# Optimization experiments

Measured on AMD Instinct MI355X. Metric: run time of the kernel, lower is better.

Reference implementation:

```python
import jax, jax.numpy as jnp
import numpy as np
from jax import lax

RESO = 64
PAD = 0.1
PLANES = ('xz', 'xy', 'yz')
_AX = {'xz': (0, 2), 'xy': (0, 1), 'yz': (1, 2)}


def _normalize(p, plane):
    a, b = _AX[plane]
    xy = jnp.stack([p[..., a], p[..., b]], axis=-1)
    xy = (xy + 0.5) / (1.0 + PAD + 1e-6)
    return jnp.clip(xy, 0.0, 1.0 - 1e-6)


def _coord2index(xy):
    xi = (xy * RESO).astype(jnp.int32)
    return xi[..., 0] + RESO * xi[..., 1]  # [B,N]


def _scatter_mean(feat, idx):  # feat [B,N,C], idx [B,N] -> [B,RESO^2,C]
    R2 = RESO * RESO
    def one(f, i):
        s = jnp.zeros((R2, f.shape[-1]), f.dtype).at[i].add(f)
        cnt = jnp.zeros((R2,), f.dtype).at[i].add(1.0)
        return s / jnp.maximum(cnt, 1.0)[:, None]
    return jax.vmap(one)(feat, idx)


def _resblock(x, W0, b0, W1, b1, Ws):
    h = jax.nn.relu(x @ W0.T + b0)
    dx = jax.nn.relu(h @ W1.T + b1)
    return x @ Ws.T + dx


def _conv(x, W, b):
    y = lax.conv_general_dilated(x, W, (1, 1), 'SAME', dimension_numbers=('NCHW', 'OIHW', 'NCHW'))
    return y + b[None, :, None, None]


def _grid_sample_border(fea, grid):
    # fea [B,C,H,W], grid [B,N,2] with (x->W, y->H) in [-1,1]; bilinear, border padding, align_corners=False
    B, C, H, W = fea.shape
    x = jnp.clip(((grid[..., 0] + 1.0) * W - 1.0) * 0.5, 0.0, W - 1.0)
    y = jnp.clip(((grid[..., 1] + 1.0) * H - 1.0) * 0.5, 0.0, H - 1.0)
    x0 = jnp.floor(x); y0 = jnp.floor(y)
    wx = (x - x0)[:, None, :]; wy = (y - y0)[:, None, :]
    x0i = x0.astype(jnp.int32); y0i = y0.astype(jnp.int32)
    x1i = jnp.minimum(x0i + 1, W - 1); y1i = jnp.minimum(y0i + 1, H - 1)
    flat = fea.reshape(B, C, H * W)
    g = lambda yi, xi: jnp.take_along_axis(flat, (yi * W + xi)[:, None, :], axis=2)  # [B,C,N]
    return (g(y0i, x0i) * (1 - wx) * (1 - wy) + g(y0i, x1i) * wx * (1 - wy)
            + g(y1i, x0i) * (1 - wx) * wy + g(y1i, x1i) * wx * wy)


def setup_inputs() -> dict:
    key = jax.random.key(0)
    ks = jax.random.split(key, 16)
    B, N, Nq, H, F = 4, 30000, 30000, 64, 256
    nrm = lambda k, sh, s: jax.random.normal(k, sh, jnp.float32) * s
    return {
        'p': jax.random.uniform(ks[0], (B, N, 3), jnp.float32, -0.5, 0.5),
        'query': jax.random.uniform(ks[1], (B, Nq, 3), jnp.float32, 0.0, 1.0),
        'fc_pos_W': nrm(ks[2], (2 * H, 3), 0.3),
        'fc_pos_b': jnp.zeros((2 * H,), jnp.float32),
        'blk_fc0_W': nrm(ks[3], (3, H, 2 * H), 0.08),
        'blk_fc0_b': jnp.zeros((3, H), jnp.float32),
        'blk_fc1_W': nrm(ks[4], (3, H, H), 0.1),
        'blk_fc1_b': jnp.zeros((3, H), jnp.float32),
        'blk_sc_W': nrm(ks[5], (3, H, 2 * H), 0.08),
        'fc_c_W': nrm(ks[6], (F, H), 0.1),
        'fc_c_b': jnp.zeros((F,), jnp.float32),
        'conv1_W': nrm(ks[7], (F, F, 3, 3), 0.02),
        'conv1_b': jnp.zeros((F,), jnp.float32),
        'conv2_W': nrm(ks[8], (F, F, 3, 3), 0.02),
        'conv2_b': jnp.zeros((F,), jnp.float32),
    }


def reference(p, query, fc_pos_W, fc_pos_b, blk_fc0_W, blk_fc0_b, blk_fc1_W, blk_fc1_b, blk_sc_W, fc_c_W, fc_c_b, conv1_W, conv1_b, conv2_W, conv2_b):
    # point-wise MLP with local pooling (scatter_mean to xz bins, gather back)
    net = p @ fc_pos_W.T + fc_pos_b                  # [B,N,2H]
    net = _resblock(net, blk_fc0_W[0], blk_fc0_b[0], blk_fc1_W[0], blk_fc1_b[0], blk_sc_W[0])  # [B,N,H]
    idx_xz = _coord2index(_normalize(p, 'xz'))       # [B,N]
    for i in (1, 2):
        binmean = _scatter_mean(net, idx_xz)         # [B,R2,H]
        pooled = jnp.take_along_axis(binmean, idx_xz[..., None], axis=1)  # [B,N,H]
        net = jnp.concatenate([net, pooled], axis=-1)
        net = _resblock(net, blk_fc0_W[i], blk_fc0_b[i], blk_fc1_W[i], blk_fc1_b[i], blk_sc_W[i])
    c = net @ fc_c_W.T + fc_c_b                      # [B,N,F]

    B = p.shape[0]
    F = fc_c_W.shape[0]
    out = 0.0
    for plane in PLANES:
        idx = _coord2index(_normalize(p, plane))
        fea = _scatter_mean(c, idx)                  # [B,R2,F]
        fea = fea.transpose(0, 2, 1).reshape(B, F, RESO, RESO)  # H axis = coord1, W axis = coord0
        fea = jax.nn.relu(_conv(fea, conv1_W, conv1_b))
        fea = jax.nn.relu(_conv(fea, conv2_W, conv2_b))
        a, b = _AX[plane]
        grid = jnp.stack([query[..., a], query[..., b]], axis=-1) * 2.0 - 1.0
        out = out + _grid_sample_border(fea, grid)   # [B,F,Nq]
    return out.transpose(0, 2, 1)                    # [B,Nq,F]
```

## Files before the change

### kernel.cpp

```cpp
#include <hip/hip_runtime.h>

#define NPTS 30000
#define PSTR 30208
#define BB 4
#define R2 4096
#define NIMG 12

typedef __attribute__((ext_vector_type(8))) short short8;
typedef __attribute__((ext_vector_type(4))) float floatx4;

__device__ __forceinline__ ushort f2bf(float x){
    union { float f; unsigned u; } v; v.f = x;
    unsigned r = (v.u + 0x7fffu + ((v.u >> 16) & 1u)) >> 16;
    return (ushort)r;
}
__device__ __forceinline__ float bf2f(ushort u){
    union { unsigned u; float f; } v; v.u = ((unsigned)u) << 16; return v.f;
}
__device__ __forceinline__ int p64i(int k){ return (k & 3)*16 + (k >> 2); }

__device__ __forceinline__ int coord_bin(float v){
    float t = (v + 0.5f) / 1.100001f;
    t = fminf(fmaxf(t, 0.0f), 0.999999f);
    return (int)(t * 64.0f);
}

__device__ __forceinline__ void gl_lds16(const ushort* g, ushort* l){
    __builtin_amdgcn_global_load_lds(
        (const __attribute__((address_space(1))) void*)g,
        (__attribute__((address_space(3))) void*)l, 16, 0, 0);
}

__global__ void k_prep(const float* __restrict__ fc_pos_W, const float* __restrict__ fc_pos_b,
                       const float* __restrict__ blk0W, const float* __restrict__ blk1W,
                       const float* __restrict__ blkSW, const float* __restrict__ fccW,
                       const float* __restrict__ c1W, const float* __restrict__ c2W,
                       float* __restrict__ WposTp, float* __restrict__ bposP,
                       ushort* __restrict__ Wcat, ushort* __restrict__ W1p,
                       ushort* __restrict__ Wcp,
                       ushort* __restrict__ WB1, ushort* __restrict__ WB2){
    int t = blockIdx.x*256 + threadIdx.x;
    if (t < 384){ int d = t/128, s = t%128;
        int j = (s<64)? p64i(s) : 64 + p64i(s-64);
        WposTp[t] = fc_pos_W[j*3 + d]; return; }
    t -= 384;
    if (t < 128){ int j = (t<64)? p64i(t) : 64 + p64i(t-64);
        bposP[t] = fc_pos_b[j]; return; }
    t -= 128;
    if (t < 49152){
        int i = t/16384, r = t%16384, n = r/128, kp = r%128;
        int ci = (kp<64)? p64i(kp) : 64 + p64i(kp-64);
        float v = (n<64)? blk0W[(i*64+n)*128 + ci] : blkSW[(i*64+(n-64))*128 + ci];
        Wcat[t] = f2bf(v); return; }
    t -= 49152;
    if (t < 12288){
        int i = t/4096, r = t%4096, n = r/64, kp = r%64;
        W1p[t] = f2bf(blk1W[(i*64+n)*64 + p64i(kp)]); return; }
    t -= 12288;
    if (t < 16384){
        int n = t/64, kp = t%64;
        Wcp[t] = f2bf(fccW[n*64 + p64i(kp)]); return; }
    t -= 16384;
    if (t < 589824){
        int e = t & 7; int rest = t >> 3; int ko = rest & 255; int g5 = rest >> 8;
        int qq = g5 & 3; int kc = (g5 >> 2) & 1; int cc = (g5 >> 3) & 3; int tap = g5 >> 5;
        int kp = cc*64 + kc*32 + qq*8 + e;
        int ci = 64*(kp>>6) + p64i(kp & 63);
        WB1[t] = f2bf(c1W[(ko*256+ci)*9 + tap]); return; }
    t -= 589824;
    if (t < 589824){
        int e = t & 7; int rest = t >> 3; int ko = rest & 255; int g5 = rest >> 8;
        int qq = g5 & 3; int kc = (g5 >> 2) & 1; int cc = (g5 >> 3) & 3; int tap = g5 >> 5;
        int kp = cc*64 + kc*32 + qq*8 + e;
        WB2[t] = f2bf(c2W[(ko*256+kp)*9 + tap]); return; }
}

__global__ void k_net0(const float* __restrict__ p, const float* __restrict__ WposTp,
                       const float* __restrict__ bposP,
                       ushort* __restrict__ NET0, int* __restrict__ IDX){
    int pt = blockIdx.x*256 + threadIdx.x;
    int b = blockIdx.y;
    if (pt >= NPTS) return;
    const float* pp = p + ((long)b*NPTS + pt)*3;
    float p0 = pp[0], p1 = pp[1], p2 = pp[2];
    int c0 = coord_bin(p0), c1 = coord_bin(p1), c2 = coord_bin(p2);
    IDX[(0*BB + b)*NPTS + pt] = c0 + 64*c2;
    IDX[(1*BB + b)*NPTS + pt] = c0 + 64*c1;
    IDX[(2*BB + b)*NPTS + pt] = c1 + 64*c2;
    ushort* out = NET0 + ((long)b*PSTR + pt)*128;
    #pragma unroll
    for (int s = 0; s < 128; s += 4){
        ushort4 v;
        v.x = f2bf(bposP[s+0] + p0*WposTp[s+0] + p1*WposTp[128+s+0] + p2*WposTp[256+s+0]);
        v.y = f2bf(bposP[s+1] + p0*WposTp[s+1] + p1*WposTp[128+s+1] + p2*WposTp[256+s+1]);
        v.z = f2bf(bposP[s+2] + p0*WposTp[s+2] + p1*WposTp[128+s+2] + p2*WposTp[256+s+2]);
        v.w = f2bf(bposP[s+3] + p0*WposTp[s+3] + p1*WposTp[128+s+3] + p2*WposTp[256+s+3]);
        *(ushort4*)(out + s) = v;
    }
}

__global__ void k_qbin(const float* __restrict__ query, int* __restrict__ qIDX){
    int t = blockIdx.x*256 + threadIdx.x;
    if (t >= BB*NPTS) return;
    const float* qp = query + (long)t*3;
    int x = min((int)(fmaxf(qp[0], 0.0f)*16.0f), 15);
    int y = min((int)(fmaxf(qp[1], 0.0f)*16.0f), 15);
    int z = min((int)(fmaxf(qp[2], 0.0f)*16.0f), 15);
    qIDX[t] = (x<<8) | (y<<4) | z;
}

__global__ void k_hist(const int* __restrict__ IDX, int* __restrict__ hist, int n){
    int t = blockIdx.x*256 + threadIdx.x;
    if (t >= n) return;
    int img = t / NPTS;
    atomicAdd(&hist[img*R2 + IDX[t]], 1);
}

__global__ void k_scan(const int* __restrict__ hist, int* __restrict__ binStart,
                       int* __restrict__ cursor){
    __shared__ int sums[256];
    int img = blockIdx.x; int tid = threadIdx.x;
    int v[16]; int s = 0;
    const int* h = hist + img*R2 + tid*16;
    #pragma unroll
    for (int i=0;i<16;i++){ v[i] = s; s += h[i]; }
    sums[tid] = s;
    __syncthreads();
    for (int d=1; d<256; d<<=1){
        int t = (tid>=d)? sums[tid-d] : 0;
        __syncthreads();
        sums[tid] += t;
        __syncthreads();
    }
    int base = (tid==0)? 0 : sums[tid-1];
    int* bs = binStart + img*R2 + tid*16;
    int* cu = cursor  + img*R2 + tid*16;
    #pragma unroll
    for (int i=0;i<16;i++){ bs[i] = base + v[i]; cu[i] = base + v[i]; }
}

__global__ void k_mklist(const int* __restrict__ IDX, int* __restrict__ cursor,
                         int* __restrict__ plist, int n){
    int t = blockIdx.x*256 + threadIdx.x;
    if (t >= n) return;
    int img = t / NPTS; int pt = t - img*NPTS;
    int bin = IDX[t];
    int pos = atomicAdd(&cursor[img*R2 + bin], 1);
    plist[img*NPTS + pos] = pt;
}

__global__ void __launch_bounds__(256) k_res_mfma(
        const ushort* __restrict__ X1, const ushort* __restrict__ X2, int s1, int s2,
        const ushort* __restrict__ Wcat, const float* __restrict__ b0,
        const ushort* __restrict__ W1p, const float* __restrict__ b1,
        ushort* __restrict__ Y){
    __shared__ __align__(16) ushort lds[4][64*72];
    int tid = threadIdx.x, lane = tid & 63, w = tid >> 6;
    int m16 = lane & 15, q = lane >> 4;
    int b = blockIdx.y;
    int pt0 = blockIdx.x*256 + w*64;
    const ushort* x1 = X1 + (long)b*PSTR*s1;
    const ushort* x2 = X2 + (long)b*PSTR*s2;
    floatx4 accH[4][4], accS[4][4];
    #pragma unroll
    for (int nt=0; nt<4; nt++){
        float bv = b0[nt*16 + m16];
        #pragma unroll
        for (int mt=0; mt<4; mt++){
            floatx4 t = {bv,bv,bv,bv}; accH[mt][nt] = t;
            floatx4 z = {0.f,0.f,0.f,0.f}; accS[mt][nt] = z;
        }
    }
    #pragma unroll
    for (int kk=0; kk<4; kk++){
        const ushort* xs = (kk<2)? x1 : x2;
        int st = (kk<2)? s1 : s2;
        int off = (kk&1)*32 + q*8;
        short8 a[4], bh[4], bs[4];
        #pragma unroll
        for (int mt=0; mt<4; mt++)
            a[mt] = *(const short8*)(xs + (long)(pt0 + mt*16 + m16)*st + off);
        #pragma unroll
        for (int nt=0; nt<4; nt++){
            bh[nt] = *(const short8*)(Wcat + (nt*16 + m16)*128 + kk*32 + q*8);
            bs[nt] = *(const short8*)(Wcat + ((nt+4)*16 + m16)*128 + kk*32 + q*8);
        }
        #pragma unroll
        for (int mt=0; mt<4; mt++)
            #pragma unroll
            for (int nt=0; nt<4; nt++){
                accH[mt][nt] = __builtin_amdgcn_mfma_f32_16x16x32_bf16(a[mt], bh[nt], accH[mt][nt], 0,0,0);
                accS[mt][nt] = __builtin_amdgcn_mfma_f32_16x16x32_bf16(a[mt], bs[nt], accS[mt][nt], 0,0,0);
            }
    }
    ushort* myl = lds[w];
    #pragma unroll
    for (int mt=0; mt<4; mt++)
        #pragma unroll
        for (int r=0; r<4; r++){
            int ptl = mt*16 + q*4 + r;
            ushort4 hv;
            hv.x = f2bf(fmaxf(accH[mt][0][r], 0.0f));
            hv.y = f2bf(fmaxf(accH[mt][1][r], 0.0f));
            hv.z = f2bf(fmaxf(accH[mt][2][r], 0.0f));
            hv.w = f2bf(fmaxf(accH[mt][3][r], 0.0f));
            *(ushort4*)&myl[ptl*72 + m16*4] = hv;
        }
    floatx4 accD[4][4];
    #pragma unroll
    for (int nt=0; nt<4; nt++){
        float bv = b1[nt*16 + m16];
        #pragma unroll
        for (int mt=0; mt<4; mt++){ floatx4 t = {bv,bv,bv,bv}; accD[mt][nt] = t; }
    }
    #pragma unroll
    for (int kk=0; kk<2; kk++){
        short8 a[4], bb[4];
        #pragma unroll
        for (int mt=0; mt<4; mt++)
            a[mt] = *(const short8*)&myl[(mt*16 + m16)*72 + kk*32 + q*8];
        #pragma unroll
        for (int nt=0; nt<4; nt++)
            bb[nt] = *(const short8*)(W1p + (nt*16 + m16)*64 + kk*32 + q*8);
        #pragma unroll
        for (int mt=0; mt<4; mt++)
            #pragma unroll
            for (int nt=0; nt<4; nt++)
                accD[mt][nt] = __builtin_amdgcn_mfma_f32_16x16x32_bf16(a[mt], bb[nt], accD[mt][nt], 0,0,0);
    }
    #pragma unroll
    for (int mt=0; mt<4; mt++)
        #pragma unroll
        for (int r=0; r<4; r++){
            int pt = pt0 + mt*16 + q*4 + r;
            if (pt < NPTS){
                ushort4 yv;
                yv.x = f2bf(accS[mt][0][r] + fmaxf(accD[mt][0][r], 0.0f));
                yv.y = f2bf(accS[mt][1][r] + fmaxf(accD[mt][1][r], 0.0f));
                yv.z = f2bf(accS[mt][2][r] + fmaxf(accD[mt][2][r], 0.0f));
                yv.w = f2bf(accS[mt][3][r] + fmaxf(accD[mt][3][r], 0.0f));
                *(ushort4*)(Y + ((long)b*PSTR + pt)*64 + m16*4) = yv;
            }
        }
}

__global__ void k_poolgather(const ushort* __restrict__ Y, const int* __restrict__ plist,
                             const int* __restrict__ binStart, const int* __restrict__ hist,
                             ushort* __restrict__ POOL){
    int tid = threadIdx.x; int lane = tid & 63; int wv = tid >> 6;
    int g = blockIdx.x*4 + wv;
    int b = g >> 12; int bl = g & 4095;
    int idx = b*R2 + bl;
    int start = binStart[idx]; int cnt = hist[idx];
    const int* pl = plist + b*NPTS;
    float s = 0.0f;
    for (int i=0;i<cnt;i++){
        int pt = pl[start+i];
        s += bf2f(Y[((long)b*PSTR + pt)*64 + lane]);
    }
    ushort sv = f2bf(s / fmaxf((float)cnt, 1.0f));
    for (int i=0;i<cnt;i++){
        int pt = pl[start+i];
        POOL[((long)b*PSTR + pt)*64 + lane] = sv;
    }
}

__global__ void k_gather64(const ushort* __restrict__ Y, const int* __restrict__ plist,
                           const int* __restrict__ binStart, const int* __restrict__ hist,
                           ushort* __restrict__ BIN){
    int tid = threadIdx.x; int lane = tid & 63; int wv = tid >> 6;
    int g = blockIdx.x*4 + wv;
    int img = g >> 12; int bl = g & 4095;
    int b = img & 3;
    int idx = img*R2 + bl;
    int start = binStart[idx]; int cnt = hist[idx];
    const int* pl = plist + img*NPTS;
    const ushort* Yb = Y + (long)b*PSTR*64 + lane;
    float s = 0.0f;
    for (int i=0;i<cnt;i++){
        int pt = pl[start+i];
        s += bf2f(Yb[(long)pt*64]);
    }
    BIN[(long)g*64 + lane] = f2bf(s / fmaxf((float)cnt, 1.0f));
}

__global__ void __launch_bounds__(256) k_fc_bins(const ushort* __restrict__ BIN,
        const ushort* __restrict__ Wcp, const float* __restrict__ bc,
        const int* __restrict__ hist, ushort* __restrict__ G){
    int tid = threadIdx.x, lane = tid & 63, w = tid >> 6;
    int m16 = lane & 15, q = lane >> 4;
    int r0 = blockIdx.x*64;
    int n0 = w*64;
    floatx4 acc[4][4];
    #pragma unroll
    for (int nt=0; nt<4; nt++){
        float bv = bc[n0 + nt*16 + m16];
        #pragma unroll
        for (int mt=0; mt<4; mt++){ floatx4 t = {bv,bv,bv,bv}; acc[mt][nt] = t; }
    }
    #pragma unroll
    for (int kk=0; kk<2; kk++){
        short8 a[4], bb[4];
        #pragma unroll
        for (int mt=0; mt<4; mt++)
            a[mt] = *(const short8*)(BIN + (long)(r0 + mt*16 + m16)*64 + kk*32 + q*8);
        #pragma unroll
        for (int nt=0; nt<4; nt++)
            bb[nt] = *(const short8*)(Wcp + (n0 + nt*16 + m16)*64 + kk*32 + q*8);
        #pragma unroll
        for (int mt=0; mt<4; mt++)
            #pragma unroll
            for (int nt=0; nt<4; nt++)
                acc[mt][nt] = __builtin_amdgcn_mfma_f32_16x16x32_bf16(a[mt], bb[nt], acc[mt][nt], 0,0,0);
    }
    #pragma unroll
    for (int mt=0; mt<4; mt++)
        #pragma unroll
        for (int r=0; r<4; r++){
            int row = r0 + mt*16 + q*4 + r;
            int cnt = hist[row];
            ushort4 v;
            if (cnt > 0){
                v.x = f2bf(acc[mt][0][r]); v.y = f2bf(acc[mt][1][r]);
                v.z = f2bf(acc[mt][2][r]); v.w = f2bf(acc[mt][3][r]);
            } else {
                v.x = 0; v.y = 0; v.z = 0; v.w = 0;
            }
            *(ushort4*)(G + (long)row*256 + n0 + m16*4) = v;
        }
}

__global__ void __launch_bounds__(256, 3) k_conv_mfma(const ushort* __restrict__ IN,
        const ushort* __restrict__ WBt, const float* __restrict__ bias, ushort* __restrict__ OUT){
    __shared__ __align__(16) ushort lds[2][3*66*64];
    int tid = threadIdx.x;
    int lane = tid & 63;
    int w = tid >> 6;
    int n0 = __builtin_amdgcn_readfirstlane(w * 64);
    int bid = blockIdx.x;
    int wg = (bid & 7) * 96 + (bid >> 3);
    int img = wg >> 6;
    int y = wg & 63;
    const ushort* inb = IN + (long)img*4096*256;
    int m16 = lane & 15, q = lane >> 4;

    if (tid < 96){
        int st = tid & 7; int c = tid >> 3;
        int buf = c / 6; int rr = (c % 6) >> 1; int colh = (c & 1) * 65;
        short8 z = {0,0,0,0,0,0,0,0};
        *(short8*)&lds[buf][(rr*66 + colh)*64 + st*8] = z;
    }

    floatx4 acc[4][4];
    #pragma unroll
    for (int j=0;j<4;j++){
        float bv = bias[n0 + 16*j + m16];
        #pragma unroll
        for (int i=0;i<4;i++){ floatx4 t = {bv,bv,bv,bv}; acc[i][j] = t; }
    }

    int sgx = lane >> 3;
    int sst = lane & 7;
    int sg  = sst ^ ((1 + sgx) & 7);

    auto stage = [&](int buf, int cc){
        #pragma unroll
        for (int r3 = 0; r3 < 3; ++r3){
            int gy = y + r3 - 1;
            if (gy < 0 || gy > 63) continue;
            const ushort* grow = inb + (long)gy*64*256 + cc*64 + sg*8;
            #pragma unroll
            for (int t = 0; t < 2; ++t){
                int col8 = w + t*4;
                const ushort* gp = grow + (long)(col8*8 + sgx)*256;
                ushort* lp = &lds[buf][(r3*66 + 1 + col8*8)*64];
                gl_lds16(gp, lp);
            }
        }
    };

    auto compute = [&](int buf, int cc){
        const ushort* lb = &lds[buf][0];
        #pragma unroll
        for (int r3 = 0; r3 < 3; ++r3){
            int gy = y + r3 - 1;
            if (gy < 0 || gy > 63) continue;
            #pragma unroll
            for (int s = 0; s < 3; ++s){
                int tap = r3*3 + s;
                #pragma unroll
                for (int kc = 0; kc < 2; ++kc){
                    short8 a[4], b[4];
                    #pragma unroll
                    for (int j=0;j<4;j++)
                        b[j] = *(const short8*)(WBt + (long)(tap*32 + cc*8 + kc*4 + q)*2048
                                                    + (n0 + 16*j + m16)*8);
                    #pragma unroll
                    for (int i=0;i<4;i++){
                        int colh = 16*i + m16 + s;
                        int sl = (kc*4 + q) ^ (colh & 7);
                        a[i] = *(const short8*)(lb + (r3*66 + colh)*64 + sl*8);
                    }
                    #pragma unroll
                    for (int i=0;i<4;i++)
                        #pragma unroll
                        for (int j=0;j<4;j++)
                            acc[i][j] = __builtin_amdgcn_mfma_f32_16x16x32_bf16(a[i], b[j], acc[i][j], 0, 0, 0);
                }
            }
        }
    };

    stage(0, 0);
    __syncthreads();
    #pragma unroll 1
    for (int cc = 0; cc < 4; ++cc){
        if (cc < 3) stage((cc+1)&1, cc+1);
        compute(cc&1, cc);
        __syncthreads();
    }

    long base = ((long)img*4096 + (long)y*64);
    #pragma unroll
    for (int i=0;i<4;i++){
        #pragma unroll
        for (int rr=0;rr<4;rr++){
            int px = 16*i + q*4 + rr;
            long rowoff = (base + px)*256;
            #pragma unroll
            for (int j=0;j<4;j++){
                float v = fmaxf(acc[i][j][rr], 0.0f);
                OUT[rowoff + n0 + 16*j + m16] = f2bf(v);
            }
        }
    }
}

__global__ void k_sample(const ushort* __restrict__ A2, const float* __restrict__ query,
                         const int* __restrict__ qlist, float* __restrict__ out){
    int lane = threadIdx.x & 63;
    int g = blockIdx.x*4 + (threadIdx.x >> 6);
    int b = blockIdx.y;
    int q = qlist[b*NPTS + g];
    const float* qp = query + ((long)b*NPTS + q)*3;
    float q0 = qp[0], q1 = qp[1], q2 = qp[2];
    float a0 = 0.f, a1 = 0.f, a2v = 0.f, a3 = 0.f;
    #pragma unroll
    for (int pl = 0; pl < 3; pl++){
        float qa = (pl==2) ? q1 : q0;
        float qb = (pl==1) ? q1 : q2;
        float gx = qa*2.0f - 1.0f, gy = qb*2.0f - 1.0f;
        float xf = ((gx + 1.0f)*64.0f - 1.0f)*0.5f;
        float yf = ((gy + 1.0f)*64.0f - 1.0f)*0.5f;
        xf = fminf(fmaxf(xf, 0.0f), 63.0f);
        yf = fminf(fmaxf(yf, 0.0f), 63.0f);
        float x0f = floorf(xf), y0f = floorf(yf);
        float wx = xf - x0f, wy = yf - y0f;
        int x0 = (int)x0f, y0 = (int)y0f;
        int x1 = min(x0+1, 63), y1 = min(y0+1, 63);
        const ushort* base = A2 + ((long)(pl*BB+b)*R2)*256 + lane*4;
        ushort4 t00 = *(const ushort4*)(base + (long)(y0*64+x0)*256);
        ushort4 t01 = *(const ushort4*)(base + (long)(y0*64+x1)*256);
        ushort4 t10 = *(const ushort4*)(base + (long)(y1*64+x0)*256);
        ushort4 t11 = *(const ushort4*)(base + (long)(y1*64+x1)*256);
        float w00 = (1.0f-wx)*(1.0f-wy), w01 = wx*(1.0f-wy);
        float w10 = (1.0f-wx)*wy,        w11 = wx*wy;
        a0  += bf2f(t00.x)*w00 + bf2f(t01.x)*w01 + bf2f(t10.x)*w10 + bf2f(t11.x)*w11;
        a1  += bf2f(t00.y)*w00 + bf2f(t01.y)*w01 + bf2f(t10.y)*w10 + bf2f(t11.y)*w11;
        a2v += bf2f(t00.z)*w00 + bf2f(t01.z)*w01 + bf2f(t10.z)*w10 + bf2f(t11.z)*w11;
        a3  += bf2f(t00.w)*w00 + bf2f(t01.w)*w01 + bf2f(t10.w)*w10 + bf2f(t11.w)*w11;
    }
    float4 r; r.x = a0; r.y = a1; r.z = a2v; r.w = a3;
    *(float4*)(out + ((long)b*NPTS + q)*256 + lane*4) = r;
}

extern "C" void kernel_launch(void* const* d_in, const int* in_sizes, int n_in,
                              void* d_out, int out_size, void* d_ws, size_t ws_size,
                              hipStream_t stream){
    (void)in_sizes; (void)n_in; (void)out_size; (void)ws_size;
    const float* p        = (const float*)d_in[0];
    const float* query    = (const float*)d_in[1];
    const float* fc_pos_W = (const float*)d_in[2];
    const float* fc_pos_b = (const float*)d_in[3];
    const float* blk0W    = (const float*)d_in[4];
    const float* blk0b    = (const float*)d_in[5];
    const float* blk1W    = (const float*)d_in[6];
    const float* blk1b    = (const float*)d_in[7];
    const float* blkSW    = (const float*)d_in[8];
    const float* fccW     = (const float*)d_in[9];
    const float* fccB     = (const float*)d_in[10];
    const float* c1W      = (const float*)d_in[11];
    const float* c1b      = (const float*)d_in[12];
    const float* c2W      = (const float*)d_in[13];
    const float* c2b      = (const float*)d_in[14];

    char* ws = (char*)d_ws;
    size_t off = 0;
    auto alloc = [&](size_t bytes)->char*{
        char* r = ws + off; off = (off + bytes + 255) & ~(size_t)255; return r; };
    float* WposTp = (float*)alloc(384*4);
    float* bposP  = (float*)alloc(128*4);
    ushort* Wcat  = (ushort*)alloc(49152UL*2);
    ushort* W1p   = (ushort*)alloc(12288UL*2);
    ushort* Wcp   = (ushort*)alloc(16384UL*2);
    ushort* WB1   = (ushort*)alloc(589824UL*2);
    ushort* WB2   = (ushort*)alloc(589824UL*2);
    int*   IDX   = (int*)  alloc((size_t)NIMG*NPTS*4);
    int*   qIDX  = (int*)  alloc((size_t)BB*NPTS*4);
    int*   hist  = (int*)  alloc((size_t)(NIMG+BB)*R2*4);
    int*   qhist = hist + (size_t)NIMG*R2;
    int*   binStart = (int*)alloc((size_t)NIMG*R2*4);
    int*   cursor   = (int*)alloc((size_t)NIMG*R2*4);
    int*   plist    = (int*)alloc((size_t)NIMG*NPTS*4);
    int*   qbinStart = (int*)alloc((size_t)BB*R2*4);
    int*   qcursor   = (int*)alloc((size_t)BB*R2*4);
    int*   qlist     = (int*)alloc((size_t)BB*NPTS*4);
    ushort* NET0 = (ushort*)alloc((size_t)BB*PSTR*128*2);
    ushort* Ya   = (ushort*)alloc((size_t)BB*PSTR*64*2);
    ushort* Yb   = (ushort*)alloc((size_t)BB*PSTR*64*2);
    ushort* POOL = (ushort*)alloc((size_t)BB*PSTR*64*2);
    ushort* BIN64= (ushort*)alloc((size_t)NIMG*R2*64*2);
    ushort* G    = (ushort*)alloc(12582912UL*2);
    ushort* A1   = (ushort*)alloc(12582912UL*2);
    ushort* A2   = (ushort*)alloc(12582912UL*2);

    dim3 blk(256);
    k_prep<<<4914, blk, 0, stream>>>(fc_pos_W, fc_pos_b, blk0W, blk1W, blkSW, fccW, c1W, c2W,
                                     WposTp, bposP, Wcat, W1p, Wcp, WB1, WB2);
    k_net0<<<dim3(118, BB), blk, 0, stream>>>(p, WposTp, bposP, NET0, IDX);
    k_qbin<<<(BB*NPTS + 255)/256, blk, 0, stream>>>(query, qIDX);
    hipMemsetAsync(hist, 0, (size_t)(NIMG+BB)*R2*4, stream);
    k_hist  <<<(NIMG*NPTS + 255)/256, blk, 0, stream>>>(IDX, hist, NIMG*NPTS);
    k_hist  <<<(BB*NPTS + 255)/256, blk, 0, stream>>>(qIDX, qhist, BB*NPTS);
    k_scan  <<<NIMG, blk, 0, stream>>>(hist, binStart, cursor);
    k_scan  <<<BB,   blk, 0, stream>>>(qhist, qbinStart, qcursor);
    k_mklist<<<(NIMG*NPTS + 255)/256, blk, 0, stream>>>(IDX, cursor, plist, NIMG*NPTS);
    k_mklist<<<(BB*NPTS + 255)/256, blk, 0, stream>>>(qIDX, qcursor, qlist, BB*NPTS);
    k_res_mfma<<<dim3(118,BB), blk, 0, stream>>>(NET0, NET0 + 64, 128, 128,
                                                 Wcat, blk0b, W1p, blk1b, Ya);
    k_poolgather<<<4096, blk, 0, stream>>>(Ya, plist, binStart, hist, POOL);
    k_res_mfma<<<dim3(118,BB), blk, 0, stream>>>(Ya, POOL, 64, 64,
                                                 Wcat + 16384, blk0b + 64, W1p + 4096, blk1b + 64, Yb);
    k_poolgather<<<4096, blk, 0, stream>>>(Yb, plist, binStart, hist, POOL);
    k_res_mfma<<<dim3(118,BB), blk, 0, stream>>>(Yb, POOL, 64, 64,
                                                 Wcat + 32768, blk0b + 128, W1p + 8192, blk1b + 128, Ya);
    k_gather64<<<12288, blk, 0, stream>>>(Ya, plist, binStart, hist, BIN64);
    k_fc_bins<<<768, blk, 0, stream>>>(BIN64, Wcp, fccB, hist, G);
    k_conv_mfma<<<dim3(768), blk, 0, stream>>>(G,  WB1, c1b, A1);
    k_conv_mfma<<<dim3(768), blk, 0, stream>>>(A1, WB2, c2b, A2);
    k_sample<<<dim3(7500,BB), blk, 0, stream>>>(A2, query, qlist, (float*)d_out);
}
```

Before: 523.3 us.

## Read pooled bin means directly in resblock and merge query sort passes

The pool-gather kernel no longer scatters each bin mean back to every point. It now writes a compact per-bin mean table, and the resblock kernel gathers its second input from that table using each point's bin index. Query binning moves into the point-encoding kernel, so the histogram, scan and list-building passes run once over 16 images instead of twice. This cuts a full-size per-point write and several launches, at the cost of indirect, less coalesced reads inside the MFMA kernel.

```diff
diff --git a/kernel.cpp b/kernel.cpp
--- a/kernel.cpp
+++ b/kernel.cpp
@@ -5,6 +5,7 @@
 #define BB 4
 #define R2 4096
 #define NIMG 12
+#define NSORT 16
 
 typedef __attribute__((ext_vector_type(8))) short short8;
 typedef __attribute__((ext_vector_type(4))) float floatx4;
@@ -75,8 +76,8 @@
         WB2[t] = f2bf(c2W[(ko*256+kp)*9 + tap]); return; }
 }
 
-__global__ void k_net0(const float* __restrict__ p, const float* __restrict__ WposTp,
-                       const float* __restrict__ bposP,
+__global__ void k_net0(const float* __restrict__ p, const float* __restrict__ query,
+                       const float* __restrict__ WposTp, const float* __restrict__ bposP,
                        ushort* __restrict__ NET0, int* __restrict__ IDX){
     int pt = blockIdx.x*256 + threadIdx.x;
     int b = blockIdx.y;
@@ -87,6 +88,11 @@
     IDX[(0*BB + b)*NPTS + pt] = c0 + 64*c2;
     IDX[(1*BB + b)*NPTS + pt] = c0 + 64*c1;
     IDX[(2*BB + b)*NPTS + pt] = c1 + 64*c2;
+    const float* qp = query + ((long)b*NPTS + pt)*3;
+    int qx = min((int)(fmaxf(qp[0], 0.0f)*16.0f), 15);
+    int qy = min((int)(fmaxf(qp[1], 0.0f)*16.0f), 15);
+    int qz = min((int)(fmaxf(qp[2], 0.0f)*16.0f), 15);
+    IDX[(12 + b)*NPTS + pt] = (qx<<8) | (qy<<4) | qz;
     ushort* out = NET0 + ((long)b*PSTR + pt)*128;
     #pragma unroll
     for (int s = 0; s < 128; s += 4){
@@ -97,16 +103,6 @@
         v.w = f2bf(bposP[s+3] + p0*WposTp[s+3] + p1*WposTp[128+s+3] + p2*WposTp[256+s+3]);
         *(ushort4*)(out + s) = v;
     }
-}
-
-__global__ void k_qbin(const float* __restrict__ query, int* __restrict__ qIDX){
-    int t = blockIdx.x*256 + threadIdx.x;
-    if (t >= BB*NPTS) return;
-    const float* qp = query + (long)t*3;
-    int x = min((int)(fmaxf(qp[0], 0.0f)*16.0f), 15);
-    int y = min((int)(fmaxf(qp[1], 0.0f)*16.0f), 15);
-    int z = min((int)(fmaxf(qp[2], 0.0f)*16.0f), 15);
-    qIDX[t] = (x<<8) | (y<<4) | z;
 }
 
 __global__ void k_hist(const int* __restrict__ IDX, int* __restrict__ hist, int n){
@@ -149,8 +145,10 @@
     plist[img*NPTS + pos] = pt;
 }
 
+template<bool POOLED>
 __global__ void __launch_bounds__(256) k_res_mfma(
         const ushort* __restrict__ X1, const ushort* __restrict__ X2, int s1, int s2,
+        const int* __restrict__ idxp,
         const ushort* __restrict__ Wcat, const float* __restrict__ b0,
         const ushort* __restrict__ W1p, const float* __restrict__ b1,
         ushort* __restrict__ Y){
@@ -160,7 +158,13 @@
     int b = blockIdx.y;
     int pt0 = blockIdx.x*256 + w*64;
     const ushort* x1 = X1 + (long)b*PSTR*s1;
-    const ushort* x2 = X2 + (long)b*PSTR*s2;
+    const ushort* x2 = POOLED ? (X2 + (long)b*R2*64) : (X2 + (long)b*PSTR*s2);
+    int bi[4];
+    if (POOLED){
+        const int* ip = idxp + (long)b*NPTS;
+        #pragma unroll
+        for (int mt=0; mt<4; mt++) bi[mt] = ip[pt0 + mt*16 + m16];
+    }
     floatx4 accH[4][4], accS[4][4];
     #pragma unroll
     for (int nt=0; nt<4; nt++){
@@ -173,13 +177,16 @@
     }
     #pragma unroll
     for (int kk=0; kk<4; kk++){
-        const ushort* xs = (kk<2)? x1 : x2;
-        int st = (kk<2)? s1 : s2;
         int off = (kk&1)*32 + q*8;
         short8 a[4], bh[4], bs[4];
         #pragma unroll
-        for (int mt=0; mt<4; mt++)
-            a[mt] = *(const short8*)(xs + (long)(pt0 + mt*16 + m16)*st + off);
+        for (int mt=0; mt<4; mt++){
+            const ushort* ap;
+            if (kk < 2)       ap = x1 + (long)(pt0 + mt*16 + m16)*s1 + off;
+            else if (POOLED)  ap = x2 + (long)bi[mt]*64 + off;
+            else              ap = x2 + (long)(pt0 + mt*16 + m16)*s2 + off;
+            a[mt] = *(const short8*)ap;
+        }
         #pragma unroll
         for (int nt=0; nt<4; nt++){
             bh[nt] = *(const short8*)(Wcat + (nt*16 + m16)*128 + kk*32 + q*8);
@@ -244,25 +251,22 @@
         }
 }
 
-__global__ void k_poolgather(const ushort* __restrict__ Y, const int* __restrict__ plist,
-                             const int* __restrict__ binStart, const int* __restrict__ hist,
-                             ushort* __restrict__ POOL){
+__global__ void k_binmean(const ushort* __restrict__ Y, const int* __restrict__ plist,
+                          const int* __restrict__ binStart, const int* __restrict__ hist,
+                          ushort* __restrict__ BINP){
     int tid = threadIdx.x; int lane = tid & 63; int wv = tid >> 6;
     int g = blockIdx.x*4 + wv;
     int b = g >> 12; int bl = g & 4095;
     int idx = b*R2 + bl;
     int start = binStart[idx]; int cnt = hist[idx];
     const int* pl = plist + b*NPTS;
+    const ushort* Yb = Y + (long)b*PSTR*64 + lane;
     float s = 0.0f;
     for (int i=0;i<cnt;i++){
         int pt = pl[start+i];
-        s += bf2f(Y[((long)b*PSTR + pt)*64 + lane]);
-    }
-    ushort sv = f2bf(s / fmaxf((float)cnt, 1.0f));
-    for (int i=0;i<cnt;i++){
-        int pt = pl[start+i];
-        POOL[((long)b*PSTR + pt)*64 + lane] = sv;
-    }
+        s += bf2f(Yb[(long)pt*64]);
+    }
+    BINP[(long)idx*64 + lane] = f2bf(s / fmaxf((float)cnt, 1.0f));
 }
 
 __global__ void k_gather64(const ushort* __restrict__ Y, const int* __restrict__ plist,
@@ -505,20 +509,15 @@
     ushort* Wcp   = (ushort*)alloc(16384UL*2);
     ushort* WB1   = (ushort*)alloc(589824UL*2);
     ushort* WB2   = (ushort*)alloc(589824UL*2);
-    int*   IDX   = (int*)  alloc((size_t)NIMG*NPTS*4);
-    int*   qIDX  = (int*)  alloc((size_t)BB*NPTS*4);
-    int*   hist  = (int*)  alloc((size_t)(NIMG+BB)*R2*4);
-    int*   qhist = hist + (size_t)NIMG*R2;
-    int*   binStart = (int*)alloc((size_t)NIMG*R2*4);
-    int*   cursor   = (int*)alloc((size_t)NIMG*R2*4);
-    int*   plist    = (int*)alloc((size_t)NIMG*NPTS*4);
-    int*   qbinStart = (int*)alloc((size_t)BB*R2*4);
-    int*   qcursor   = (int*)alloc((size_t)BB*R2*4);
-    int*   qlist     = (int*)alloc((size_t)BB*NPTS*4);
+    int*   IDX   = (int*)  alloc((size_t)NSORT*NPTS*4);
+    int*   hist  = (int*)  alloc((size_t)NSORT*R2*4);
+    int*   binStart = (int*)alloc((size_t)NSORT*R2*4);
+    int*   cursor   = (int*)alloc((size_t)NSORT*R2*4);
+    int*   plist    = (int*)alloc((size_t)NSORT*NPTS*4);
     ushort* NET0 = (ushort*)alloc((size_t)BB*PSTR*128*2);
     ushort* Ya   = (ushort*)alloc((size_t)BB*PSTR*64*2);
     ushort* Yb   = (ushort*)alloc((size_t)BB*PSTR*64*2);
-    ushort* POOL = (ushort*)alloc((size_t)BB*PSTR*64*2);
+    ushort* BINP = (ushort*)alloc((size_t)BB*R2*64*2);
     ushort* BIN64= (ushort*)alloc((size_t)NIMG*R2*64*2);
     ushort* G    = (ushort*)alloc(12582912UL*2);
     ushort* A1   = (ushort*)alloc(12582912UL*2);
@@ -527,26 +526,22 @@
     dim3 blk(256);
     k_prep<<<4914, blk, 0, stream>>>(fc_pos_W, fc_pos_b, blk0W, blk1W, blkSW, fccW, c1W, c2W,
                                      WposTp, bposP, Wcat, W1p, Wcp, WB1, WB2);
-    k_net0<<<dim3(118, BB), blk, 0, stream>>>(p, WposTp, bposP, NET0, IDX);
-    k_qbin<<<(BB*NPTS + 255)/256, blk, 0, stream>>>(query, qIDX);
-    hipMemsetAsync(hist, 0, (size_t)(NIMG+BB)*R2*4, stream);
-    k_hist  <<<(NIMG*NPTS + 255)/256, blk, 0, stream>>>(IDX, hist, NIMG*NPTS);
-    k_hist  <<<(BB*NPTS + 255)/256, blk, 0, stream>>>(qIDX, qhist, BB*NPTS);
-    k_scan  <<<NIMG, blk, 0, stream>>>(hist, binStart, cursor);
-    k_scan  <<<BB,   blk, 0, stream>>>(qhist, qbinStart, qcursor);
-    k_mklist<<<(NIMG*NPTS + 255)/256, blk, 0, stream>>>(IDX, cursor, plist, NIMG*NPTS);
-    k_mklist<<<(BB*NPTS + 255)/256, blk, 0, stream>>>(qIDX, qcursor, qlist, BB*NPTS);
-    k_res_mfma<<<dim3(118,BB), blk, 0, stream>>>(NET0, NET0 + 64, 128, 128,
+    k_net0<<<dim3(118, BB), blk, 0, stream>>>(p, query, WposTp, bposP, NET0, IDX);
+    hipMemsetAsync(hist, 0, (size_t)NSORT*R2*4, stream);
+    k_hist  <<<(NSORT*NPTS + 255)/256, blk, 0, stream>>>(IDX, hist, NSORT*NPTS);
+    k_scan  <<<NSORT, blk, 0, stream>>>(hist, binStart, cursor);
+    k_mklist<<<(NSORT*NPTS + 255)/256, blk, 0, stream>>>(IDX, cursor, plist, NSORT*NPTS);
+    k_res_mfma<false><<<dim3(118,BB), blk, 0, stream>>>(NET0, NET0 + 64, 128, 128, nullptr,
                                                  Wcat, blk0b, W1p, blk1b, Ya);
-    k_poolgather<<<4096, blk, 0, stream>>>(Ya, plist, binStart, hist, POOL);
-    k_res_mfma<<<dim3(118,BB), blk, 0, stream>>>(Ya, POOL, 64, 64,
+    k_binmean<<<4096, blk, 0, stream>>>(Ya, plist, binStart, hist, BINP);
+    k_res_mfma<true><<<dim3(118,BB), blk, 0, stream>>>(Ya, BINP, 64, 64, IDX,
                                                  Wcat + 16384, blk0b + 64, W1p + 4096, blk1b + 64, Yb);
-    k_poolgather<<<4096, blk, 0, stream>>>(Yb, plist, binStart, hist, POOL);
-    k_res_mfma<<<dim3(118,BB), blk, 0, stream>>>(Yb, POOL, 64, 64,
+    k_binmean<<<4096, blk, 0, stream>>>(Yb, plist, binStart, hist, BINP);
+    k_res_mfma<true><<<dim3(118,BB), blk, 0, stream>>>(Yb, BINP, 64, 64, IDX,
                                                  Wcat + 32768, blk0b + 128, W1p + 8192, blk1b + 128, Ya);
     k_gather64<<<12288, blk, 0, stream>>>(Ya, plist, binStart, hist, BIN64);
     k_fc_bins<<<768, blk, 0, stream>>>(BIN64, Wcp, fccB, hist, G);
     k_conv_mfma<<<dim3(768), blk, 0, stream>>>(G,  WB1, c1b, A1);
     k_conv_mfma<<<dim3(768), blk, 0, stream>>>(A1, WB2, c2b, A2);
-    k_sample<<<dim3(7500,BB), blk, 0, stream>>>(A2, query, qlist, (float*)d_out);
-}
+    k_sample<<<dim3(7500,BB), blk, 0, stream>>>(A2, query, plist + 12*NPTS, (float*)d_out);
+}
```

Result: faster. 507.8 us (-3.0%).
